# Kernel optimization log

Hardware: AMD Instinct MI355X
Metric: run time of the kernel (lower is better)

## Reference

```python
import jax, jax.numpy as jnp
import numpy as np

B, N, M, K, D, DO = 4, 32768, 8192, 16, 128, 128


def setup_inputs() -> dict:
    key = jax.random.key(0)
    ks = jax.random.split(key, 8)
    return dict(
        xyz=jax.random.normal(ks[0], (B, N, 3), jnp.float32),
        x=jax.random.normal(ks[1], (B, D, N), jnp.float32),
        xyz_center=jax.random.normal(ks[2], (B, M, 3), jnp.float32),
        idx=jax.random.randint(ks[3], (B, M, K), 0, N, jnp.int32),
        alpha=jnp.ones((1,), jnp.float32),
        beta=jnp.ones((1,), jnp.float32),
        norm_radius=jnp.ones((1,), jnp.float32),
        w1=jax.random.normal(ks[4], (K, 3), jnp.float32) * 0.1,
        g1=jnp.ones((K,), jnp.float32),
        b1=jnp.zeros((K,), jnp.float32),
        w2=jax.random.normal(ks[5], (K, 2 * K), jnp.float32) * 0.1,
        g2=jnp.ones((K,), jnp.float32),
        b2=jnp.zeros((K,), jnp.float32),
        w3=jax.random.normal(ks[6], (K, 2 * K), jnp.float32) * 0.1,
        cv_w=jax.random.normal(ks[7], (DO, D, K), jnp.float32) * 0.02,
    )


def _inorm(t, g, b, eps=1e-5):
    # InstanceNorm2d: normalize each (batch, channel) plane over spatial dims (m, k)
    mu = t.mean(axis=(2, 3), keepdims=True)
    var = t.var(axis=(2, 3), keepdims=True)
    return (t - mu) * jax.lax.rsqrt(var + eps) * g[None, :, None, None] + b[None, :, None, None]


def reference(xyz, x, xyz_center, idx, alpha, beta, norm_radius, w1, g1, b1, w2, g2, b2, w3, cv_w):
    k = idx.shape[-1]
    gather = jax.vmap(lambda pts, i: pts[i])  # per-batch gather
    xyz_group = gather(xyz, idx)                      # b m k 3
    x_group = gather(jnp.swapaxes(x, 1, 2), idx)      # b m k d

    pts = xyz_group - xyz_center[:, :, None, :]       # b m k 3
    # dist computed on detached pts (torch .detach())
    dist = jnp.sqrt(jnp.sum(jnp.square(jax.lax.stop_gradient(pts)), -1))  # b m k
    mean_radius = dist.max(-1).mean()
    nr = norm_radius * 0.9 + mean_radius * 0.1        # EMA-updated radius (non-trainable)
    pts = pts / nr

    dw = jax.nn.sigmoid(-alpha * dist + beta)         # b m k
    s = dw.sum(-1, keepdims=True)
    s = s + (s == 0).astype(dw.dtype) + 1e-6
    dw = dw / s * k
    dw4 = dw[:, None, :, :]                           # b 1 m k

    ptsT = jnp.transpose(pts, (0, 3, 1, 2))           # b 3 m k
    mat = jax.nn.relu(_inorm(jnp.einsum('bcmk,oc->bomk', ptsT, w1), g1, b1))
    mp1 = jnp.broadcast_to((mat * dw4).max(-1, keepdims=True), mat.shape)
    mat = jax.nn.relu(_inorm(jnp.einsum('bcmk,oc->bomk', jnp.concatenate([mat, mp1], 1), w2), g2, b2))
    mp2 = jnp.broadcast_to((mat * dw4).max(-1, keepdims=True), mat.shape)
    mat = jax.nn.relu(jnp.einsum('bcmk,oc->bomk', jnp.concatenate([mat, mp2], 1), w3)) * dw4

    out = jnp.einsum('bmkd,bjmk->bdmj', x_group, mat)  # b d m k
    out = jnp.einsum('bdmj,odj->bom', out, cv_w)
    return out
```

## Files before the change

### kernel.cpp

```cpp
#include <hip/hip_runtime.h>
#include <hip/hip_bf16.h>

#define BB 4
#define NN 32768
#define MM 8192
#define KK 16
#define DD 128
#define DOUT 128
#define TT 2048

typedef unsigned short ushortT;
typedef unsigned int uintT;
typedef __attribute__((ext_vector_type(8))) short short8;
typedef __attribute__((ext_vector_type(4))) float f32x4;
typedef __attribute__((ext_vector_type(2))) float f32x2;

__device__ __forceinline__ ushortT f2bf(float f) {
  union { float f; uintT u; } v; v.f = f;
  uintT u = v.u;
  return (ushortT)((u + 0x7FFFu + ((u >> 16) & 1u)) >> 16);
}

#define ST_MAXD 0
#define ST_E1 16
#define ST_A1 160
#define ST_B1 224
#define ST_E2 288
#define ST_A2 416
#define ST_B2 480

__global__ __launch_bounds__(256) void kxT(const float* __restrict__ x, ushortT* __restrict__ xTb) {
  __shared__ float tile[32][33];
  const int b = blockIdx.z;
  const int n0 = blockIdx.x * 32, d0 = blockIdx.y * 32;
  const int tx = threadIdx.x, ty = threadIdx.y;
  const float* xp = x + (size_t)b * DD * NN;
  #pragma unroll
  for (int i = 0; i < 4; i++)
    tile[ty + i * 8][tx] = xp[(size_t)(d0 + ty + i * 8) * NN + n0 + tx];
  __syncthreads();
  ushortT* op = xTb + (size_t)b * NN * DD;
  #pragma unroll
  for (int i = 0; i < 4; i++)
    op[(size_t)(n0 + ty + i * 8) * DD + d0 + tx] = f2bf(tile[tx][ty + i * 8]);
}

__global__ __launch_bounds__(256) void kWb(const float* __restrict__ cw, ushortT* __restrict__ wb) {
  const int i = blockIdx.x * 256 + threadIdx.x;
  wb[i] = f2bf(cw[i]);
}

__global__ __launch_bounds__(256) void kpassA(const float* __restrict__ xyz,
    const float* __restrict__ xyzc, const int* __restrict__ idx,
    const float* __restrict__ w1, float* __restrict__ st, float4* __restrict__ pts4) {
  const int b = blockIdx.y;
  const int tid = threadIdx.x;
  const int mloc = tid >> 4, k = tid & 15;
  const int m = blockIdx.x * 16 + mloc;
  const int gi = (b * MM + m) * KK + k;
  const int n = idx[gi];
  const float cx = xyzc[(b * MM + m) * 3 + 0];
  const float cy = xyzc[(b * MM + m) * 3 + 1];
  const float cz = xyzc[(b * MM + m) * 3 + 2];
  const float* p = xyz + ((size_t)b * NN + n) * 3;
  const float px = p[0] - cx, py = p[1] - cy, pz = p[2] - cz;
  const float dist = sqrtf(px * px + py * py + pz * pz);
  pts4[gi] = (float4){px, py, pz, dist};
  float maxd = dist;
  maxd = fmaxf(maxd, __shfl_xor(maxd, 1));
  maxd = fmaxf(maxd, __shfl_xor(maxd, 2));
  maxd = fmaxf(maxd, __shfl_xor(maxd, 4));
  maxd = fmaxf(maxd, __shfl_xor(maxd, 8));
  __shared__ float red[16];
  __shared__ float wred[4][32];
  if (k == 0) red[mloc] = maxd;
  float vs[16], vq[16];
  #pragma unroll
  for (int o = 0; o < 16; o++) {
    float e = px * w1[3 * o] + py * w1[3 * o + 1] + pz * w1[3 * o + 2];
    vs[o] = e; vq[o] = e * e;
  }
  #pragma unroll
  for (int s = 1; s < 64; s <<= 1) {
    #pragma unroll
    for (int o = 0; o < 16; o++) {
      vs[o] += __shfl_xor(vs[o], s);
      vq[o] += __shfl_xor(vq[o], s);
    }
  }
  const int wv = tid >> 6, lane = tid & 63;
  if (lane == 0) {
    #pragma unroll
    for (int o = 0; o < 16; o++) { wred[wv][o] = vs[o]; wred[wv][16 + o] = vq[o]; }
  }
  __syncthreads();
  if (tid < 32) {
    float a = wred[0][tid] + wred[1][tid] + wred[2][tid] + wred[3][tid];
    atomicAdd(&st[ST_E1 + b * 32 + tid], a);
  }
  if (tid == 0) {
    float s = 0.f;
    #pragma unroll
    for (int i = 0; i < 16; i++) s += red[i];
    atomicAdd(&st[ST_MAXD], s);
  }
}

__global__ void kS1(const float* __restrict__ nrad, const float* __restrict__ g1,
                    const float* __restrict__ b1, float* __restrict__ st) {
  const int tid = threadIdx.x;
  if (tid >= 64) return;
  const float meanrad = st[ST_MAXD] / (float)(BB * MM);
  const float nr = nrad[0] * 0.9f + meanrad * 0.1f;
  const int b = tid >> 4, o = tid & 15;
  const float cnt = (float)(MM * KK);
  const float sum = st[ST_E1 + b * 32 + o];
  const float sq  = st[ST_E1 + b * 32 + 16 + o];
  const float mu = sum / cnt;
  float var = sq / cnt - mu * mu; var = fmaxf(var, 0.f);
  const float invs = rsqrtf(var + 1e-5f * nr * nr);
  const float a = invs * g1[o];
  st[ST_A1 + b * 16 + o] = a;
  st[ST_B1 + b * 16 + o] = b1[o] - mu * a;
}

__global__ __launch_bounds__(256) void kpassB(const float4* __restrict__ pts4,
    const float* __restrict__ alpha, const float* __restrict__ beta,
    const float* __restrict__ w1, const float* __restrict__ w2,
    float* __restrict__ st) {
  const int b = blockIdx.y;
  const int tid = threadIdx.x;
  __shared__ float w2s[512];
  __shared__ float wred[4][32];
  w2s[tid] = w2[tid]; w2s[256 + tid] = w2[256 + tid];
  const int gi = b * MM * KK + blockIdx.x * 256 + tid;
  const float4 p4 = pts4[gi];
  const float px = p4.x, py = p4.y, pz = p4.z, dist = p4.w;
  float dwv = 1.f / (1.f + expf(alpha[0] * dist - beta[0]));
  float s = dwv;
  s += __shfl_xor(s, 1); s += __shfl_xor(s, 2); s += __shfl_xor(s, 4); s += __shfl_xor(s, 8);
  s = s + (s == 0.f ? 1.f : 0.f) + 1e-6f;
  dwv = dwv / s * 16.f;
  float mat1[16], mp1[16];
  #pragma unroll
  for (int o = 0; o < 16; o++) {
    float e = px * w1[3 * o] + py * w1[3 * o + 1] + pz * w1[3 * o + 2];
    float v = e * st[ST_A1 + b * 16 + o] + st[ST_B1 + b * 16 + o];
    mat1[o] = fmaxf(v, 0.f);
    float t = mat1[o] * dwv;
    t = fmaxf(t, __shfl_xor(t, 1)); t = fmaxf(t, __shfl_xor(t, 2));
    t = fmaxf(t, __shfl_xor(t, 4)); t = fmaxf(t, __shfl_xor(t, 8));
    mp1[o] = t;
  }
  __syncthreads();
  float vs[16], vq[16];
  #pragma unroll
  for (int o = 0; o < 16; o++) {
    float acc = 0.f;
    #pragma unroll
    for (int c = 0; c < 16; c++)
      acc += mat1[c] * w2s[o * 32 + c] + mp1[c] * w2s[o * 32 + 16 + c];
    vs[o] = acc; vq[o] = acc * acc;
  }
  #pragma unroll
  for (int s2 = 1; s2 < 64; s2 <<= 1) {
    #pragma unroll
    for (int o = 0; o < 16; o++) {
      vs[o] += __shfl_xor(vs[o], s2);
      vq[o] += __shfl_xor(vq[o], s2);
    }
  }
  const int wv = tid >> 6, lane = tid & 63;
  if (lane == 0) {
    #pragma unroll
    for (int o = 0; o < 16; o++) { wred[wv][o] = vs[o]; wred[wv][16 + o] = vq[o]; }
  }
  __syncthreads();
  if (tid < 32) {
    float a = wred[0][tid] + wred[1][tid] + wred[2][tid] + wred[3][tid];
    atomicAdd(&st[ST_E2 + b * 32 + tid], a);
  }
}

__global__ void kS2(const float* __restrict__ g2, const float* __restrict__ b2,
                    float* __restrict__ st) {
  const int tid = threadIdx.x;
  if (tid >= 64) return;
  const int b = tid >> 4, o = tid & 15;
  const float cnt = (float)(MM * KK);
  const float sum = st[ST_E2 + b * 32 + o];
  const float sq  = st[ST_E2 + b * 32 + 16 + o];
  const float mu = sum / cnt;
  float var = sq / cnt - mu * mu; var = fmaxf(var, 0.f);
  const float invs = rsqrtf(var + 1e-5f);
  const float a = invs * g2[o];
  st[ST_A2 + b * 16 + o] = a;
  st[ST_B2 + b * 16 + o] = b2[o] - mu * a;
}

__global__ __launch_bounds__(512, 4) void kF1(const float4* __restrict__ pts4,
    const int* __restrict__ idx,
    const float* __restrict__ alpha, const float* __restrict__ beta,
    const float* __restrict__ w1, const float* __restrict__ w2, const float* __restrict__ w3,
    const float* __restrict__ st, const ushortT* __restrict__ xTb, ushortT* __restrict__ Aout) {
  __shared__ float w2s[512], w3s[512];
  __shared__ float mat3s[32 * 320];
  __shared__ int nls[512];
  const int b = blockIdx.y;
  const int tid = threadIdx.x;
  const int m0 = blockIdx.x * 32;
  w2s[tid] = w2[tid];
  w3s[tid] = w3[tid];

  const int mloc = tid >> 4, k1 = tid & 15;
  const int gi = (b * MM + m0) * KK + tid;
  nls[tid] = idx[gi];
  const float4 p4 = pts4[gi];
  const float px = p4.x, py = p4.y, pz = p4.z, dist = p4.w;
  float dwv = 1.f / (1.f + expf(alpha[0] * dist - beta[0]));
  {
    float s = dwv;
    s += __shfl_xor(s, 1); s += __shfl_xor(s, 2); s += __shfl_xor(s, 4); s += __shfl_xor(s, 8);
    s = s + (s == 0.f ? 1.f : 0.f) + 1e-6f;
    dwv = dwv / s * 16.f;
  }
  float mat1[16], mp1[16];
  #pragma unroll
  for (int o = 0; o < 16; o++) {
    float e = px * w1[3 * o] + py * w1[3 * o + 1] + pz * w1[3 * o + 2];
    float v = e * st[ST_A1 + b * 16 + o] + st[ST_B1 + b * 16 + o];
    mat1[o] = fmaxf(v, 0.f);
    float t = mat1[o] * dwv;
    t = fmaxf(t, __shfl_xor(t, 1)); t = fmaxf(t, __shfl_xor(t, 2));
    t = fmaxf(t, __shfl_xor(t, 4)); t = fmaxf(t, __shfl_xor(t, 8));
    mp1[o] = t;
  }
  __syncthreads();
  {
    float mat2[16], mp2[16];
    #pragma unroll
    for (int o = 0; o < 16; o++) {
      float acc = 0.f;
      #pragma unroll
      for (int c = 0; c < 16; c++)
        acc += mat1[c] * w2s[o * 32 + c] + mp1[c] * w2s[o * 32 + 16 + c];
      float v = acc * st[ST_A2 + b * 16 + o] + st[ST_B2 + b * 16 + o];
      mat2[o] = fmaxf(v, 0.f);
      float t = mat2[o] * dwv;
      t = fmaxf(t, __shfl_xor(t, 1)); t = fmaxf(t, __shfl_xor(t, 2));
      t = fmaxf(t, __shfl_xor(t, 4)); t = fmaxf(t, __shfl_xor(t, 8));
      mp2[o] = t;
    }
    float* m3w = &mat3s[mloc * 320 + k1 * 20];
    #pragma unroll
    for (int j = 0; j < 16; j++) {
      float acc = 0.f;
      #pragma unroll
      for (int c = 0; c < 16; c++)
        acc += mat2[c] * w3s[j * 32 + c] + mp2[c] * w3s[j * 32 + 16 + c];
      m3w[j] = fmaxf(acc, 0.f) * dwv;
    }
  }
  __syncthreads();

  const int dl = tid & 31;
  const int d0 = dl * 4;
  const ushortT* xb = xTb + (size_t)b * NN * DD + d0;
  #pragma unroll 1
  for (int g = 0; g < 2; g++) {
    const int ml = g * 16 + (tid >> 5);
    const float* m3base = &mat3s[ml * 320];
    const int* nbase = &nls[ml * 16];
    f32x2 a2[4][8];
    #pragma unroll
    for (int d = 0; d < 4; d++)
      #pragma unroll
      for (int c = 0; c < 8; c++) a2[d][c] = (f32x2){0.f, 0.f};
    #pragma unroll 4
    for (int k = 0; k < 16; k++) {
      const int nn = nbase[k];
      const uint2 xv = *(const uint2*)(xb + (size_t)nn * DD);
      float xs[4];
      xs[0] = __uint_as_float(xv.x << 16);
      xs[1] = __uint_as_float(xv.x & 0xFFFF0000u);
      xs[2] = __uint_as_float(xv.y << 16);
      xs[3] = __uint_as_float(xv.y & 0xFFFF0000u);
      const f32x4 m30 = *(const f32x4*)(m3base + k * 20 + 0);
      const f32x4 m31 = *(const f32x4*)(m3base + k * 20 + 4);
      const f32x4 m32 = *(const f32x4*)(m3base + k * 20 + 8);
      const f32x4 m33 = *(const f32x4*)(m3base + k * 20 + 12);
      f32x2 mp[8];
      mp[0] = m30.lo; mp[1] = m30.hi;
      mp[2] = m31.lo; mp[3] = m31.hi;
      mp[4] = m32.lo; mp[5] = m32.hi;
      mp[6] = m33.lo; mp[7] = m33.hi;
      #pragma unroll
      for (int d = 0; d < 4; d++) {
        const float xd = xs[d];
        #pragma unroll
        for (int c = 0; c < 8; c++)
          a2[d][c] += mp[c] * xd;
      }
    }
    ushortT* aop = Aout + ((size_t)b * MM + m0 + ml) * TT + d0 * 16;
    #pragma unroll
    for (int d = 0; d < 4; d++) {
      uintT u[8];
      #pragma unroll
      for (int i = 0; i < 8; i++)
        u[i] = (uintT)f2bf(a2[d][i].x) | ((uintT)f2bf(a2[d][i].y) << 16);
      uint4* dst = (uint4*)(aop + d * 16);
      dst[0] = (uint4){u[0], u[1], u[2], u[3]};
      dst[1] = (uint4){u[4], u[5], u[6], u[7]};
    }
  }
}

__global__ __launch_bounds__(512) void kgemm(const ushortT* __restrict__ Wb,
                                             const ushortT* __restrict__ Aout,
                                             float* __restrict__ out) {
  __shared__ ushortT At[128 * 40];
  __shared__ ushortT Bt[128 * 40];
  const int b = blockIdx.y;
  const int m0 = blockIdx.x * 128;
  const int tid = threadIdx.x;
  const int w = tid >> 6, l = tid & 63;
  const int ow = (w >> 2) * 64, mw = (w & 3) * 32;
  const int fr = l & 15, fg = l >> 4;
  f32x4 acc[4][2];
  #pragma unroll
  for (int i = 0; i < 4; i++)
    #pragma unroll
    for (int j = 0; j < 2; j++)
      acc[i][j] = (f32x4){0.f, 0.f, 0.f, 0.f};
  const int srow = tid >> 2, sk = (tid & 3) * 8;
  const ushortT* wp = Wb + srow * TT + sk;
  const ushortT* ap = Aout + ((size_t)b * MM + m0 + srow) * TT + sk;
  for (int k0 = 0; k0 < TT; k0 += 32) {
    uint4 wv = *(const uint4*)(wp + k0);
    uint4 av = *(const uint4*)(ap + k0);
    *(uint4*)&At[srow * 40 + sk] = wv;
    *(uint4*)&Bt[srow * 40 + sk] = av;
    __syncthreads();
    short8 a[4], bfrag[2];
    #pragma unroll
    for (int i = 0; i < 4; i++) a[i] = *(short8*)&At[(ow + i * 16 + fr) * 40 + fg * 8];
    #pragma unroll
    for (int j = 0; j < 2; j++) bfrag[j] = *(short8*)&Bt[(mw + j * 16 + fr) * 40 + fg * 8];
    #pragma unroll
    for (int i = 0; i < 4; i++)
      #pragma unroll
      for (int j = 0; j < 2; j++)
        acc[i][j] = __builtin_amdgcn_mfma_f32_16x16x32_bf16(a[i], bfrag[j], acc[i][j], 0, 0, 0);
    __syncthreads();
  }
  #pragma unroll
  for (int i = 0; i < 4; i++)
    #pragma unroll
    for (int j = 0; j < 2; j++)
      #pragma unroll
      for (int r = 0; r < 4; r++) {
        const int o = ow + i * 16 + fg * 4 + r;
        const int m = m0 + mw + j * 16 + fr;
        out[((size_t)b * DOUT + o) * MM + m] = acc[i][j][r];
      }
}

#define XTB_OFF 0
#define PTS_OFF 33554432
#define AOUT_OFF 67108864
#define WB_OFF 201326592
#define ST_OFF 201850880

extern "C" void kernel_launch(void* const* d_in, const int* in_sizes, int n_in,
                              void* d_out, int out_size, void* d_ws, size_t ws_size,
                              hipStream_t stream) {
  const float* xyz  = (const float*)d_in[0];
  const float* x    = (const float*)d_in[1];
  const float* xyzc = (const float*)d_in[2];
  const int*   idx  = (const int*)d_in[3];
  const float* alpha = (const float*)d_in[4];
  const float* beta  = (const float*)d_in[5];
  const float* nrad  = (const float*)d_in[6];
  const float* w1 = (const float*)d_in[7];
  const float* g1 = (const float*)d_in[8];
  const float* b1 = (const float*)d_in[9];
  const float* w2 = (const float*)d_in[10];
  const float* g2 = (const float*)d_in[11];
  const float* b2 = (const float*)d_in[12];
  const float* w3 = (const float*)d_in[13];
  const float* cvw = (const float*)d_in[14];
  char* ws = (char*)d_ws;
  ushortT* xTb  = (ushortT*)(ws + XTB_OFF);
  float4*  pts4 = (float4*)(ws + PTS_OFF);
  ushortT* Aout = (ushortT*)(ws + AOUT_OFF);
  ushortT* Wb   = (ushortT*)(ws + WB_OFF);
  float*   st   = (float*)(ws + ST_OFF);
  float* out = (float*)d_out;

  hipMemsetAsync(st, 0, 4096, stream);
  kxT<<<dim3(NN / 32, DD / 32, BB), dim3(32, 8), 0, stream>>>(x, xTb);
  kWb<<<dim3(DOUT * TT / 256), 256, 0, stream>>>(cvw, Wb);
  kpassA<<<dim3(MM / 16, BB), 256, 0, stream>>>(xyz, xyzc, idx, w1, st, pts4);
  kS1<<<1, 64, 0, stream>>>(nrad, g1, b1, st);
  kpassB<<<dim3(MM / 16, BB), 256, 0, stream>>>(pts4, alpha, beta, w1, w2, st);
  kS2<<<1, 64, 0, stream>>>(g2, b2, st);
  kF1<<<dim3(MM / 32, BB), 512, 0, stream>>>(pts4, idx, alpha, beta, w1, w2, w3, st, xTb, Aout);
  kgemm<<<dim3(MM / 128, BB), 512, 0, stream>>>(Wb, Aout, out);
}
```

Baseline: 233.9 us.

## Split output channels across half-waves, swizzle mat3 LDS and shrink neighbor indices

The gather-contract phase of kF1 now splits the 16 output channels between the two half-waves of each wavefront. Each thread keeps 16 fp32 accumulators instead of 32, and the m-loop runs 4 times instead of 2. mat3 is stored unpadded with an XOR swizzle on 16-byte chunks to avoid LDS bank conflicts, and neighbor indices are stored as 16-bit in shared memory. The goal is to cut registers and LDS so launch bounds can ask for 8 blocks per CU. The cost is twice as many global gathers of x rows per output, because each half-wave loads the same x values.

```diff
diff --git a/kernel.cpp b/kernel.cpp
--- a/kernel.cpp
+++ b/kernel.cpp
@@ -198,14 +198,14 @@
   st[ST_B2 + b * 16 + o] = b2[o] - mu * a;
 }
 
-__global__ __launch_bounds__(512, 4) void kF1(const float4* __restrict__ pts4,
+__global__ __launch_bounds__(512, 8) void kF1(const float4* __restrict__ pts4,
     const int* __restrict__ idx,
     const float* __restrict__ alpha, const float* __restrict__ beta,
     const float* __restrict__ w1, const float* __restrict__ w2, const float* __restrict__ w3,
     const float* __restrict__ st, const ushortT* __restrict__ xTb, ushortT* __restrict__ Aout) {
   __shared__ float w2s[512], w3s[512];
-  __shared__ float mat3s[32 * 320];
-  __shared__ int nls[512];
+  __shared__ float mat3s[32 * 256];
+  __shared__ ushortT nls[512];
   const int b = blockIdx.y;
   const int tid = threadIdx.x;
   const int m0 = blockIdx.x * 32;
@@ -214,7 +214,7 @@
 
   const int mloc = tid >> 4, k1 = tid & 15;
   const int gi = (b * MM + m0) * KK + tid;
-  nls[tid] = idx[gi];
+  nls[tid] = (ushortT)idx[gi];
   const float4 p4 = pts4[gi];
   const float px = p4.x, py = p4.y, pz = p4.z, dist = p4.w;
   float dwv = 1.f / (1.f + expf(alpha[0] * dist - beta[0]));
@@ -251,67 +251,72 @@
       t = fmaxf(t, __shfl_xor(t, 4)); t = fmaxf(t, __shfl_xor(t, 8));
       mp2[o] = t;
     }
-    float* m3w = &mat3s[mloc * 320 + k1 * 20];
+    const int swz1 = (k1 ^ (k1 >> 2)) & 3;
+    float* m3w = &mat3s[mloc * 256 + k1 * 16];
+    float m3v[16];
     #pragma unroll
     for (int j = 0; j < 16; j++) {
       float acc = 0.f;
       #pragma unroll
       for (int c = 0; c < 16; c++)
         acc += mat2[c] * w3s[j * 32 + c] + mp2[c] * w3s[j * 32 + 16 + c];
-      m3w[j] = fmaxf(acc, 0.f) * dwv;
-    }
-  }
-  __syncthreads();
-
-  const int dl = tid & 31;
-  const int d0 = dl * 4;
+      m3v[j] = fmaxf(acc, 0.f) * dwv;
+    }
+    #pragma unroll
+    for (int q = 0; q < 4; q++)
+      *(f32x4*)(m3w + ((q ^ swz1) << 2)) =
+          (f32x4){m3v[4 * q], m3v[4 * q + 1], m3v[4 * q + 2], m3v[4 * q + 3]};
+  }
+  __syncthreads();
+
+  const int wid = tid >> 6;
+  const int lane = tid & 63;
+  const int jh = lane >> 5;
+  const int dq = lane & 31;
+  const int d0 = dq * 4;
+  const int jq0 = jh * 2;
   const ushortT* xb = xTb + (size_t)b * NN * DD + d0;
   #pragma unroll 1
-  for (int g = 0; g < 2; g++) {
-    const int ml = g * 16 + (tid >> 5);
-    const float* m3base = &mat3s[ml * 320];
-    const int* nbase = &nls[ml * 16];
-    f32x2 a2[4][8];
+  for (int g = 0; g < 4; g++) {
+    const int ml = g * 8 + wid;
+    const float* m3base = &mat3s[ml * 256];
+    const ushortT* nbase = &nls[ml * 16];
+    f32x2 a2[4][4];
     #pragma unroll
     for (int d = 0; d < 4; d++)
       #pragma unroll
-      for (int c = 0; c < 8; c++) a2[d][c] = (f32x2){0.f, 0.f};
+      for (int c = 0; c < 4; c++) a2[d][c] = (f32x2){0.f, 0.f};
     #pragma unroll 4
     for (int k = 0; k < 16; k++) {
+      const int sw = (k ^ (k >> 2)) & 3;
       const int nn = nbase[k];
       const uint2 xv = *(const uint2*)(xb + (size_t)nn * DD);
+      const f32x4 mq0 = *(const f32x4*)(m3base + k * 16 + ((jq0 ^ sw) << 2));
+      const f32x4 mq1 = *(const f32x4*)(m3base + k * 16 + (((jq0 + 1) ^ sw) << 2));
       float xs[4];
       xs[0] = __uint_as_float(xv.x << 16);
       xs[1] = __uint_as_float(xv.x & 0xFFFF0000u);
       xs[2] = __uint_as_float(xv.y << 16);
       xs[3] = __uint_as_float(xv.y & 0xFFFF0000u);
-      const f32x4 m30 = *(const f32x4*)(m3base + k * 20 + 0);
-      const f32x4 m31 = *(const f32x4*)(m3base + k * 20 + 4);
-      const f32x4 m32 = *(const f32x4*)(m3base + k * 20 + 8);
-      const f32x4 m33 = *(const f32x4*)(m3base + k * 20 + 12);
-      f32x2 mp[8];
-      mp[0] = m30.lo; mp[1] = m30.hi;
-      mp[2] = m31.lo; mp[3] = m31.hi;
-      mp[4] = m32.lo; mp[5] = m32.hi;
-      mp[6] = m33.lo; mp[7] = m33.hi;
+      f32x2 mp[4];
+      mp[0] = mq0.lo; mp[1] = mq0.hi;
+      mp[2] = mq1.lo; mp[3] = mq1.hi;
       #pragma unroll
       for (int d = 0; d < 4; d++) {
         const float xd = xs[d];
         #pragma unroll
-        for (int c = 0; c < 8; c++)
+        for (int c = 0; c < 4; c++)
           a2[d][c] += mp[c] * xd;
       }
     }
-    ushortT* aop = Aout + ((size_t)b * MM + m0 + ml) * TT + d0 * 16;
+    ushortT* aop = Aout + ((size_t)b * MM + m0 + ml) * TT + d0 * 16 + jh * 8;
     #pragma unroll
     for (int d = 0; d < 4; d++) {
-      uintT u[8];
-      #pragma unroll
-      for (int i = 0; i < 8; i++)
-        u[i] = (uintT)f2bf(a2[d][i].x) | ((uintT)f2bf(a2[d][i].y) << 16);
-      uint4* dst = (uint4*)(aop + d * 16);
-      dst[0] = (uint4){u[0], u[1], u[2], u[3]};
-      dst[1] = (uint4){u[4], u[5], u[6], u[7]};
+      uintT u[4];
+      #pragma unroll
+      for (int c = 0; c < 4; c++)
+        u[c] = (uintT)f2bf(a2[d][c].x) | ((uintT)f2bf(a2[d][c].y) << 16);
+      *(uint4*)(aop + d * 16) = (uint4){u[0], u[1], u[2], u[3]};
     }
   }
 }
```

Result: slower. 282.3 us (+20.7%).
